# Kernel tuning notes

Measured on AMD Instinct MI355X. Metric: run time of the kernel, lower is better.

The kernel has to match this reference:

```python
import jax, jax.numpy as jnp
import numpy as np

B, S, D, H, DFF = 4, 2048, 1024, 16, 4096
DK = D // H
EPS = 1e-6


def setup_inputs() -> dict:
    key = jax.random.key(0)
    ks = jax.random.split(key, 20)
    sc = 0.02
    inp = {
        'x': jax.random.normal(ks[0], (B, S, D), jnp.float32),
        'inp_mask': jax.random.randint(ks[1], (B, 1, 1, S), 0, 2, jnp.int32),
        # linear weights stored [in, out]
        'wq_w': jax.random.normal(ks[2], (D, D), jnp.float32) * sc,
        'wq_b': jnp.zeros((D,), jnp.float32),
        'wk_w': jax.random.normal(ks[3], (D, D), jnp.float32) * sc,
        'wk_b': jnp.zeros((D,), jnp.float32),
        'wv_w': jax.random.normal(ks[4], (D, D), jnp.float32) * sc,
        'wv_b': jnp.zeros((D,), jnp.float32),
        'wo_w': jax.random.normal(ks[5], (D, D), jnp.float32) * sc,
        'wo_b': jnp.zeros((D,), jnp.float32),
        'ff_w0': jax.random.normal(ks[6], (D, DFF), jnp.float32) * sc,
        'ff_b0': jnp.zeros((DFF,), jnp.float32),
        'ff_w1': jax.random.normal(ks[7], (DFF, D), jnp.float32) * sc,
        'ff_b1': jnp.zeros((D,), jnp.float32),
        'ln0_a': jnp.ones((D,), jnp.float32),
        'ln0_b': jnp.zeros((D,), jnp.float32),
        'ln1_a': jnp.ones((D,), jnp.float32),
        'ln1_b': jnp.zeros((D,), jnp.float32),
    }
    return inp


def _layernorm(x, alpha, bias):
    # Faithful to source: unbiased std (Bessel), divide by (std + eps)
    mean = jnp.mean(x, axis=-1, keepdims=True)
    std = jnp.std(x, axis=-1, keepdims=True, ddof=1)
    return alpha * (x - mean) / (std + EPS) + bias


def _mha(x, wq_w, wq_b, wk_w, wk_b, wv_w, wv_b, wo_w, wo_b, mask):
    q = (x @ wq_w + wq_b).reshape(B, S, H, DK).transpose(0, 2, 1, 3)  # [B,H,S,DK]
    k = (x @ wk_w + wk_b).reshape(B, S, H, DK).transpose(0, 2, 1, 3)
    v = (x @ wv_w + wv_b).reshape(B, S, H, DK).transpose(0, 2, 1, 3)
    scores = jnp.einsum('bhqd,bhkd->bhqk', q, k) / jnp.sqrt(jnp.float32(DK))
    scores = jnp.where(mask == 0, jnp.float32(-1e9), scores)
    attn = jax.nn.softmax(scores, axis=-1)
    out = jnp.einsum('bhqk,bhkd->bhqd', attn, v)
    out = out.transpose(0, 2, 1, 3).reshape(B, S, D)
    return out @ wo_w + wo_b


def reference(x, inp_mask, wq_w, wq_b, wk_w, wk_b, wv_w, wv_b, wo_w, wo_b,
              ff_w0, ff_b0, ff_w1, ff_b1, ln0_a, ln0_b, ln1_a, ln1_b):
    # Residual 0: pre-norm MHA (dropout = 0)
    h = _layernorm(x, ln0_a, ln0_b)
    x = x + _mha(h, wq_w, wq_b, wk_w, wk_b, wv_w, wv_b, wo_w, wo_b, inp_mask)
    # Residual 1: pre-norm FFN
    h = _layernorm(x, ln1_a, ln1_b)
    h = jax.nn.gelu(h @ ff_w0 + ff_b0, approximate=False) @ ff_w1 + ff_b1
    return x + h
```

## Files before the change

### kernel.cpp

```cpp
#include <hip/hip_runtime.h>
#include <hip/hip_bf16.h>
#include <math.h>

#define Bc 4
#define Sc 2048
#define Dc 1024
#define Hc 16
#define DKc 64
#define DFFc 4096
#define Mc (Bc*Sc)
#define LN_EPS 1e-6f

typedef unsigned short ushort_t;
typedef short bf16x8 __attribute__((ext_vector_type(8)));
typedef float f32x4 __attribute__((ext_vector_type(4)));
typedef float f32x16 __attribute__((ext_vector_type(16)));

typedef __attribute__((address_space(3))) void lds_void_t;
typedef __attribute__((address_space(1))) const void gconst_void_t;

__device__ __forceinline__ void gload_lds16(const void* g, void* l) {
  __builtin_amdgcn_global_load_lds((gconst_void_t*)g, (lds_void_t*)l, 16, 0, 0);
}

__device__ __forceinline__ ushort_t f2bf(float f) {
  union { float f; unsigned int u; } a; a.f = f;
  unsigned int r = a.u + 0x7fffu + ((a.u >> 16) & 1u);
  return (ushort_t)(r >> 16);
}

__device__ __forceinline__ float rcpf(float x) { return __builtin_amdgcn_rcpf(x); }

__device__ __forceinline__ void swapl(unsigned& a, unsigned& b) {
  asm("v_permlane32_swap_b32 %0, %1" : "+v"(a), "+v"(b));
}
__device__ __forceinline__ unsigned cvtpk_bf16(float lo, float hi) {
  unsigned r;
  asm("v_cvt_pk_bf16_f32 %0, %1, %2" : "=v"(r) : "v"(lo), "v"(hi));
  return r;
}

__global__ __launch_bounds__(256) void k_transpose_cvt(
    const float* __restrict__ W, ushort_t* __restrict__ WT, int K, int N) {
  __shared__ float t[32][33];
  const int tx = threadIdx.x & 31, ty = threadIdx.x >> 5;
  const int n0 = blockIdx.x * 32, k0 = blockIdx.y * 32;
#pragma unroll
  for (int i = 0; i < 4; ++i)
    t[ty + i * 8][tx] = W[(size_t)(k0 + ty + i * 8) * N + n0 + tx];
  __syncthreads();
#pragma unroll
  for (int i = 0; i < 4; ++i)
    WT[(size_t)(n0 + ty + i * 8) * K + k0 + tx] = f2bf(t[tx][ty + i * 8]);
}

__global__ __launch_bounds__(256) void k_layernorm(
    const float* __restrict__ x, const float* __restrict__ alpha,
    const float* __restrict__ beta, ushort_t* __restrict__ out) {
  const int row = blockIdx.x;
  const int tid = threadIdx.x;
  const int w = tid >> 6, lane = tid & 63;
  const float4 v = ((const float4*)(x + (size_t)row * Dc))[tid];
  float s = v.x + v.y + v.z + v.w;
#pragma unroll
  for (int m = 32; m >= 1; m >>= 1) s += __shfl_xor(s, m, 64);
  __shared__ float ws[8];
  if (lane == 0) ws[w] = s;
  __syncthreads();
  s = ws[0] + ws[1] + ws[2] + ws[3];
  const float mean = s * (1.0f / Dc);
  const float dx = v.x - mean, dy = v.y - mean, dz = v.z - mean, dw = v.w - mean;
  float ss = dx * dx + dy * dy + dz * dz + dw * dw;
#pragma unroll
  for (int m = 32; m >= 1; m >>= 1) ss += __shfl_xor(ss, m, 64);
  if (lane == 0) ws[4 + w] = ss;
  __syncthreads();
  ss = ws[4] + ws[5] + ws[6] + ws[7];
  const float stdv = sqrtf(ss / (float)(Dc - 1));
  const float inv = 1.0f / (stdv + LN_EPS);
  const float4 a = ((const float4*)alpha)[tid];
  const float4 b = ((const float4*)beta)[tid];
  uint2 o;
  o.x = cvtpk_bf16(a.x * dx * inv + b.x, a.y * dy * inv + b.y);
  o.y = cvtpk_bf16(a.z * dz * inv + b.z, a.w * dw * inv + b.w);
  *(uint2*)(out + (size_t)row * Dc + tid * 4) = o;
}

__global__ __launch_bounds__(256) void k_compact(const int* __restrict__ mask,
                                                 int* __restrict__ cidx,
                                                 float* __restrict__ cmadd,
                                                 int* __restrict__ ntile) {
  const int b = blockIdx.x;
  const int tid = threadIdx.x;
  const int base = b * Sc;
  for (int i = tid; i < Sc; i += 256) cmadd[base + i] = -1.442695041e9f;
  int mloc[8];
  int cnt = 0;
#pragma unroll
  for (int j = 0; j < 8; ++j) {
    mloc[j] = mask[base + tid * 8 + j];
    cnt += mloc[j];
  }
  __shared__ int ps[256];
  ps[tid] = cnt;
  __syncthreads();
  for (int ofs = 1; ofs < 256; ofs <<= 1) {
    const int v = (tid >= ofs) ? ps[tid - ofs] : 0;
    __syncthreads();
    ps[tid] += v;
    __syncthreads();
  }
  const int total = ps[255];
  int run = tid ? ps[tid - 1] : 0;
#pragma unroll
  for (int j = 0; j < 8; ++j) {
    const int gi = base + tid * 8 + j;
    if (mloc[j]) {
      cidx[gi] = run;
      cmadd[base + run] = -8.0f;
      run++;
    } else {
      cidx[gi] = -1;
    }
  }
  if (tid == 0) {
    int nt = (total + 31) >> 5;
    ntile[b] = nt < 1 ? 1 : nt;
  }
}

template <int MODE>
__global__ __launch_bounds__(512, 4) void k_gemm8(
    const ushort_t* __restrict__ A, const ushort_t* __restrict__ BT,
    const float* __restrict__ bias, const float* __restrict__ bias2,
    const float* __restrict__ bias3, const float* __restrict__ resid,
    const int* __restrict__ cidx,
    void* __restrict__ Cout, void* __restrict__ Cout2, void* __restrict__ Cout3,
    int N, int K, int nxn ) {
  __shared__ __align__(16) ushort_t As[3][256 * 32];
  __shared__ __align__(16) ushort_t Bs[3][128 * 32];
  const int tid = threadIdx.x;
  const int lane = tid & 63;
  const int wid = tid >> 6;
  const int wm = wid >> 1, wn = wid & 1;
  const int lrow = lane & 15, lgrp = lane >> 4;
  const int xcd = blockIdx.x & 7;
  const int idx = blockIdx.x >> 3;
  const int im = xcd * 4 + (idx & 3);
  const int in_ = idx >> 2;
  const int m0 = im << 8, n0 = in_ << 7;

  const f32x4 zero4 = {0.f, 0.f, 0.f, 0.f};
  f32x4 acc[4][4];
#pragma unroll
  for (int i = 0; i < 4; ++i)
#pragma unroll
    for (int j = 0; j < 4; ++j) acc[i][j] = zero4;

  const int ar0 = tid >> 2;
  const int as0 = (tid & 3) ^ ((ar0 >> 1) & 3);
  const int ar1 = ar0 + 128;
  const ushort_t* Ag0 = A + (size_t)(m0 + ar0) * K + as0 * 8;
  const ushort_t* Ag1 = A + (size_t)(m0 + ar1) * K + as0 * 8;
  const ushort_t* Bg0 = BT + (size_t)(n0 + ar0 % 128) * K + as0 * 8;
  char* const a_w = (char*)(&As[0][0]) + wid * 1024;
  char* const b_w = (char*)(&Bs[0][0]) + wid * 1024;

  const int sl = lgrp ^ ((lrow >> 1) & 3);
  const int aoff = (wm * 64 + lrow) * 32 + sl * 8;
  const int boff = (wn * 64 + lrow) * 32 + sl * 8;

  const int nk = K >> 5;
  {
    gload_lds16(Ag0, a_w);
    gload_lds16(Ag1, a_w + 8192);
    gload_lds16(Bg0, b_w);
    gload_lds16(Ag0 + 32, a_w + 16384);
    gload_lds16(Ag1 + 32, a_w + 16384 + 8192);
    gload_lds16(Bg0 + 32, b_w + 8192);
  }
  int cur = 0;
  for (int t = 0; t < nk; ++t) {
    if (t + 1 < nk) { asm volatile("s_waitcnt vmcnt(3)" ::: "memory"); }
    else            { asm volatile("s_waitcnt vmcnt(0)" ::: "memory"); }
    asm volatile("s_barrier" ::: "memory");
    const ushort_t* Ab = &As[cur][0];
    const ushort_t* Bb = &Bs[cur][0];
    bf16x8 af[4], bf[4];
#pragma unroll
    for (int mf = 0; mf < 4; ++mf) af[mf] = *(const bf16x8*)(Ab + aoff + mf * 512);
#pragma unroll
    for (int nf = 0; nf < 4; ++nf) bf[nf] = *(const bf16x8*)(Bb + boff + nf * 512);
    if (t + 2 < nk) {
      const int bi = (cur + 2 >= 3) ? cur - 1 : cur + 2;
      const size_t ko = (size_t)(t + 2) * 32;
      gload_lds16(Ag0 + ko, a_w + bi * 16384);
      gload_lds16(Ag1 + ko, a_w + bi * 16384 + 8192);
      gload_lds16(Bg0 + ko, b_w + bi * 8192);
    }
    __builtin_amdgcn_s_setprio(1);
#pragma unroll
    for (int mf = 0; mf < 4; ++mf)
#pragma unroll
      for (int nf = 0; nf < 4; ++nf)
        acc[mf][nf] = __builtin_amdgcn_mfma_f32_16x16x32_bf16(af[mf], bf[nf], acc[mf][nf], 0, 0, 0);
    __builtin_amdgcn_s_setprio(0);
    asm volatile("s_barrier" ::: "memory");
    cur = (cur + 1 == 3) ? 0 : cur + 1;
  }

  const float* bsrc = bias;
  int n0l = n0;
  int seg = 0;
  if (MODE == 4) {
    seg = n0 >> 10;
    n0l = n0 & 1023;
    bsrc = (seg == 0) ? bias : (seg == 1 ? bias2 : bias3);
  }
  float bv[4];
#pragma unroll
  for (int n = 0; n < 4; ++n) bv[n] = bsrc[n0l + wn * 64 + n * 16 + lrow];

  const int gb = m0 >> 11;

#pragma unroll
  for (int m = 0; m < 4; ++m) {
    int cpv[4];
    if (MODE == 4 && seg >= 1) {
#pragma unroll
      for (int r = 0; r < 4; ++r)
        cpv[r] = cidx[m0 + wm * 64 + m * 16 + lgrp * 4 + r];
    }
#pragma unroll
    for (int n = 0; n < 4; ++n) {
      const int col = (MODE == 4 ? n0l : n0) + wn * 64 + n * 16 + lrow;
      if (MODE == 4 && seg == 2) {
        const int hh = col >> 6, dd = col & 63;
        ushort_t* Cv = (ushort_t*)Cout3 + ((size_t)(gb * Hc + hh) * DKc + dd) * Sc;
#pragma unroll
        for (int r = 0; r < 4; r += 2) {
          const unsigned wpk = cvtpk_bf16(acc[m][n][r] + bv[n], acc[m][n][r + 1] + bv[n]);
          if (cpv[r] >= 0) Cv[cpv[r]] = (ushort_t)wpk;
          if (cpv[r + 1] >= 0) Cv[cpv[r + 1]] = (ushort_t)(wpk >> 16);
        }
      } else if (MODE == 4 && seg == 1) {
        ushort_t* Ck = (ushort_t*)Cout2 + (size_t)gb * Sc * Dc + col;
#pragma unroll
        for (int r = 0; r < 4; r += 2) {
          const unsigned wpk = cvtpk_bf16(acc[m][n][r] + bv[n], acc[m][n][r + 1] + bv[n]);
          if (cpv[r] >= 0) Ck[(size_t)cpv[r] * Dc] = (ushort_t)wpk;
          if (cpv[r + 1] >= 0) Ck[(size_t)cpv[r + 1] * Dc] = (ushort_t)(wpk >> 16);
        }
      } else if (MODE == 4) {
        ushort_t* Co = (ushort_t*)Cout;
        const size_t row0 = (size_t)(m0 + wm * 64 + m * 16 + lgrp * 4);
#pragma unroll
        for (int r = 0; r < 4; r += 2) {
          const unsigned wpk = cvtpk_bf16(acc[m][n][r] + bv[n], acc[m][n][r + 1] + bv[n]);
          Co[(row0 + r) * Dc + col] = (ushort_t)wpk;
          Co[(row0 + r + 1) * Dc + col] = (ushort_t)(wpk >> 16);
        }
      } else if (MODE == 2) {
        const size_t row0 = (size_t)(m0 + wm * 64 + m * 16 + lgrp * 4);
#pragma unroll
        for (int r = 0; r < 4; r += 2) {
          float v0 = acc[m][n][r] + bv[n];
          float v1 = acc[m][n][r + 1] + bv[n];
          v0 = v0 * rcpf(1.0f + exp2f(-2.4554669f * v0));
          v1 = v1 * rcpf(1.0f + exp2f(-2.4554669f * v1));
          const unsigned wpk = cvtpk_bf16(v0, v1);
          ((ushort_t*)Cout)[(row0 + r) * N + col] = (ushort_t)wpk;
          ((ushort_t*)Cout)[(row0 + r + 1) * N + col] = (ushort_t)(wpk >> 16);
        }
      } else {
#pragma unroll
        for (int r = 0; r < 4; ++r) {
          const size_t row = (size_t)(m0 + wm * 64 + m * 16 + lgrp * 4 + r);
          const float v = acc[m][n][r] + bv[n] + resid[row * N + col];
          ((float*)Cout)[row * N + col] = v;
        }
      }
    }
  }
}

#define KSCALE 0.1803368801e0f
__global__ __launch_bounds__(512) void k_attn12(
    const ushort_t* __restrict__ Qb, const ushort_t* __restrict__ Kb,
    const ushort_t* __restrict__ Vt, const float* __restrict__ madd,
    const int* __restrict__ ntile, ushort_t* __restrict__ Ob) {
  __shared__ __align__(16) ushort_t Ks[4][32 * 64];
  __shared__ __align__(16) ushort_t Vs[4][64 * 32];
  __shared__ __align__(16) float Ms[Sc];

  const int bid = blockIdx.x;
  const int xcd = bid & 7, idx = bid >> 3;
  const int bh = xcd * 8 + (idx >> 3);
  const int qb = idx & 7;
  const int b = bh >> 4, h = bh & 15;
  const int nt = ntile[b];
  const int tid = threadIdx.x;
  const int lane = tid & 63, w = tid >> 6;
  const int l31 = lane & 31, hi = lane >> 5;
  const size_t bS = (size_t)b * Sc;
  const int qrow0 = qb * 256 + w * 32;

  bf16x8 qf[4];
  const ushort_t* qp = Qb + (bS + qrow0 + l31) * Dc + h * DKc + hi * 8;
#pragma unroll
  for (int c = 0; c < 4; ++c) qf[c] = *(const bf16x8*)(qp + c * 16);

  bf16x8 ones;
#pragma unroll
  for (int i = 0; i < 8; ++i) ones[i] = (short)0x3F80;

  f32x16 accA, accB, accS;
#pragma unroll
  for (int i = 0; i < 16; ++i) { accA[i] = 0.f; accB[i] = 0.f; accS[i] = 0.f; }

  const ushort_t* Vth = Vt + (size_t)bh * (DKc * Sc);
  const float* mp = madd + b * Sc;

  const int c0 = tid & 255;
  const int kr = c0 >> 3, ksl = (c0 & 7) ^ (kr & 7);
  const int vr = c0 >> 2, vsl = (c0 & 3) ^ ((vr >> 1) & 3);
  const ushort_t* Kg = Kb + (bS + kr) * Dc + h * DKc + ksl * 8;
  const ushort_t* Vg = Vth + (size_t)vr * Sc + vsl * 8;
  char* const k_w = (char*)(&Ks[0][0]) + (w & 3) * 1024;
  char* const v_w = (char*)(&Vs[0][0]) + (w & 3) * 1024;

  gload_lds16(mp + tid * 4, (char*)Ms + w * 1024);
  if (w < 4) {
    gload_lds16(Kg, k_w);
    gload_lds16(Kg + (size_t)32 * Dc, k_w + 4096);
  } else {
    gload_lds16(Vg, v_w);
    gload_lds16(Vg + 32, v_w + 4096);
  }

  const int vsw = (l31 >> 1) & 3;
  int cur = 0;
  f32x16 scA, scB;

  auto qk_phase = [&](f32x16& scN, int t) {
    const char* Kbuf = (const char*)(&Ks[cur][0]);
    bf16x8 kf[4];
#pragma unroll
    for (int c = 0; c < 4; ++c) {
      const int slr = (c * 2 + hi) ^ (l31 & 7);
      kf[c] = *(const bf16x8*)(Kbuf + l31 * 128 + slr * 16);
    }
    if (t + 2 < 64) {
      const int bi = (cur + 2) & 3;
      const size_t kv2 = (size_t)(t + 2) * 32;
      if (w < 4) gload_lds16(Kg + kv2 * Dc, k_w + bi * 4096);
      else       gload_lds16(Vg + kv2, v_w + bi * 4096);
    }
#pragma unroll
    for (int i = 0; i < 16; ++i) scN[i] = 0.f;
    __builtin_amdgcn_s_setprio(1);
    scN = __builtin_amdgcn_mfma_f32_32x32x16_bf16(kf[0], qf[0], scN, 0, 0, 0);
    scN = __builtin_amdgcn_mfma_f32_32x32x16_bf16(kf[1], qf[1], scN, 0, 0, 0);
    scN = __builtin_amdgcn_mfma_f32_32x32x16_bf16(kf[2], qf[2], scN, 0, 0, 0);
    scN = __builtin_amdgcn_mfma_f32_32x32x16_bf16(kf[3], qf[3], scN, 0, 0, 0);
    __builtin_amdgcn_s_setprio(0);
  };

  auto sm_pv = [&](f32x16& scP, int tp) {
    float4 mv[4];
#pragma unroll
    for (int c = 0; c < 4; ++c)
      mv[c] = *(const float4*)(&Ms[tp * 32 + c * 8 + 4 * hi]);
    const char* Vbuf = (const char*)(&Vs[(cur + 3) & 3][0]);
    const bf16x8 v00 = *(const bf16x8*)(Vbuf + l31 * 64 + ((hi ^ vsw) * 16));
    const bf16x8 v01 = *(const bf16x8*)(Vbuf + l31 * 64 + (((2 + hi) ^ vsw) * 16));
    const bf16x8 v10 = *(const bf16x8*)(Vbuf + (32 + l31) * 64 + ((hi ^ vsw) * 16));
    const bf16x8 v11 = *(const bf16x8*)(Vbuf + (32 + l31) * 64 + (((2 + hi) ^ vsw) * 16));
    float p[16];
    p[0] = exp2f(scP[0] * KSCALE + mv[0].x);  p[1] = exp2f(scP[1] * KSCALE + mv[0].y);
    p[2] = exp2f(scP[2] * KSCALE + mv[0].z);  p[3] = exp2f(scP[3] * KSCALE + mv[0].w);
    p[4] = exp2f(scP[4] * KSCALE + mv[1].x);  p[5] = exp2f(scP[5] * KSCALE + mv[1].y);
    p[6] = exp2f(scP[6] * KSCALE + mv[1].z);  p[7] = exp2f(scP[7] * KSCALE + mv[1].w);
    p[8] = exp2f(scP[8] * KSCALE + mv[2].x);  p[9] = exp2f(scP[9] * KSCALE + mv[2].y);
    p[10] = exp2f(scP[10] * KSCALE + mv[2].z); p[11] = exp2f(scP[11] * KSCALE + mv[2].w);
    p[12] = exp2f(scP[12] * KSCALE + mv[3].x); p[13] = exp2f(scP[13] * KSCALE + mv[3].y);
    p[14] = exp2f(scP[14] * KSCALE + mv[3].z); p[15] = exp2f(scP[15] * KSCALE + mv[3].w);
    unsigned cw[4][2];
#pragma unroll
    for (int a = 0; a < 4; ++a) {
      cw[a][0] = cvtpk_bf16(p[4 * a + 0], p[4 * a + 1]);
      cw[a][1] = cvtpk_bf16(p[4 * a + 2], p[4 * a + 3]);
    }
    unsigned a00 = cw[0][0], b00 = cw[1][0]; swapl(a00, b00);
    unsigned a01 = cw[0][1], b01 = cw[1][1]; swapl(a01, b01);
    unsigned a10 = cw[2][0], b10 = cw[3][0]; swapl(a10, b10);
    unsigned a11 = cw[2][1], b11 = cw[3][1]; swapl(a11, b11);
    union { unsigned u[4]; bf16x8 v; } pa0, pa1;
    pa0.u[0] = a00; pa0.u[1] = a01; pa0.u[2] = b00; pa0.u[3] = b01;
    pa1.u[0] = a10; pa1.u[1] = a11; pa1.u[2] = b10; pa1.u[3] = b11;
    __builtin_amdgcn_s_setprio(1);
    accA = __builtin_amdgcn_mfma_f32_32x32x16_bf16(pa0.v, v00, accA, 0, 0, 0);
    accA = __builtin_amdgcn_mfma_f32_32x32x16_bf16(pa1.v, v01, accA, 0, 0, 0);
    accB = __builtin_amdgcn_mfma_f32_32x32x16_bf16(pa0.v, v10, accB, 0, 0, 0);
    accB = __builtin_amdgcn_mfma_f32_32x32x16_bf16(pa1.v, v11, accB, 0, 0, 0);
    accS = __builtin_amdgcn_mfma_f32_32x32x16_bf16(pa0.v, ones, accS, 0, 0, 0);
    accS = __builtin_amdgcn_mfma_f32_32x32x16_bf16(pa1.v, ones, accS, 0, 0, 0);
    __builtin_amdgcn_s_setprio(0);
  };

  asm volatile("s_waitcnt vmcnt(1)" ::: "memory");
  asm volatile("s_barrier" ::: "memory");
  qk_phase(scA, 0);
  cur = 1;
  int t = 1;
  for (; t + 1 < nt; t += 2) {
    asm volatile("s_waitcnt vmcnt(1)" ::: "memory");
    asm volatile("s_barrier" ::: "memory");
    qk_phase(scB, t);
    sm_pv(scA, t - 1);
    cur = (cur + 1) & 3;
    asm volatile("s_waitcnt vmcnt(1)" ::: "memory");
    asm volatile("s_barrier" ::: "memory");
    qk_phase(scA, t + 1);
    sm_pv(scB, t);
    cur = (cur + 1) & 3;
  }
  if (t < nt) {
    asm volatile("s_waitcnt vmcnt(1)" ::: "memory");
    asm volatile("s_barrier" ::: "memory");
    qk_phase(scB, t);
    sm_pv(scA, t - 1);
    cur = (cur + 1) & 3;
    asm volatile("s_waitcnt vmcnt(0)" ::: "memory");
    sm_pv(scB, t);
  } else {
    asm volatile("s_waitcnt vmcnt(0)" ::: "memory");
    sm_pv(scA, nt - 1);
  }

#pragma unroll
  for (int r = 0; r < 16; ++r) {
    const int q = (r & 3) + 8 * (r >> 2) + 4 * hi;
    const float inv = rcpf(accS[r]);
    ushort_t* op = Ob + (bS + qrow0 + q) * Dc + h * DKc + l31;
    op[0] = f2bf(accA[r] * inv);
    op[32] = f2bf(accB[r] * inv);
  }
}

extern "C" void kernel_launch(void* const* d_in, const int* in_sizes, int n_in,
                              void* d_out, int out_size, void* d_ws, size_t ws_size,
                              hipStream_t stream) {
  const float* x     = (const float*)d_in[0];
  const int* mask    = (const int*)d_in[1];
  const float* wq_w  = (const float*)d_in[2];
  const float* wq_b  = (const float*)d_in[3];
  const float* wk_w  = (const float*)d_in[4];
  const float* wk_b  = (const float*)d_in[5];
  const float* wv_w  = (const float*)d_in[6];
  const float* wv_b  = (const float*)d_in[7];
  const float* wo_w  = (const float*)d_in[8];
  const float* wo_b  = (const float*)d_in[9];
  const float* ff_w0 = (const float*)d_in[10];
  const float* ff_b0 = (const float*)d_in[11];
  const float* ff_w1 = (const float*)d_in[12];
  const float* ff_b1 = (const float*)d_in[13];
  const float* ln0_a = (const float*)d_in[14];
  const float* ln0_b = (const float*)d_in[15];
  const float* ln1_a = (const float*)d_in[16];
  const float* ln1_b = (const float*)d_in[17];
  float* out = (float*)d_out;

  char* ws = (char*)d_ws;
  size_t off = 0;
  ushort_t* WTq = (ushort_t*)(ws + off); off += (size_t)Dc * Dc * 2;
  ushort_t* WTk = (ushort_t*)(ws + off); off += (size_t)Dc * Dc * 2;
  ushort_t* WTv = (ushort_t*)(ws + off); off += (size_t)Dc * Dc * 2;
  ushort_t* WTo = (ushort_t*)(ws + off); off += (size_t)Dc * Dc * 2;
  ushort_t* WT0 = (ushort_t*)(ws + off); off += (size_t)DFFc * Dc * 2;
  ushort_t* WT1 = (ushort_t*)(ws + off); off += (size_t)Dc * DFFc * 2;
  ushort_t* hbuf = (ushort_t*)(ws + off); off += (size_t)Mc * Dc * 2;
  ushort_t* qbuf = (ushort_t*)(ws + off); off += (size_t)Mc * Dc * 2;
  ushort_t* kbuf = (ushort_t*)(ws + off); off += (size_t)Mc * Dc * 2;
  ushort_t* vtb  = (ushort_t*)(ws + off); off += (size_t)Mc * Dc * 2;
  ushort_t* abuf = (ushort_t*)(ws + off); off += (size_t)Mc * Dc * 2;
  float* maddb   = (float*)(ws + off);   off += (size_t)Bc * Sc * 4;
  int* cidxb     = (int*)(ws + off);     off += (size_t)Mc * 4;
  int* ntileb    = (int*)(ws + off);     off += 64;
  ushort_t* gbuf = qbuf;

  const dim3 blk(256);
  const dim3 blk512(512);
  k_transpose_cvt<<<dim3(Dc / 32, Dc / 32), blk, 0, stream>>>(wq_w, WTq, Dc, Dc);
  k_transpose_cvt<<<dim3(Dc / 32, Dc / 32), blk, 0, stream>>>(wk_w, WTk, Dc, Dc);
  k_transpose_cvt<<<dim3(Dc / 32, Dc / 32), blk, 0, stream>>>(wv_w, WTv, Dc, Dc);
  k_transpose_cvt<<<dim3(Dc / 32, Dc / 32), blk, 0, stream>>>(wo_w, WTo, Dc, Dc);
  k_transpose_cvt<<<dim3(DFFc / 32, Dc / 32), blk, 0, stream>>>(ff_w0, WT0, Dc, DFFc);
  k_transpose_cvt<<<dim3(Dc / 32, DFFc / 32), blk, 0, stream>>>(ff_w1, WT1, DFFc, Dc);
  k_compact<<<dim3(Bc), blk, 0, stream>>>(mask, cidxb, maddb, ntileb);
  k_layernorm<<<Mc, blk, 0, stream>>>(x, ln0_a, ln0_b, hbuf);
  k_gemm8<4><<<dim3(768), blk512, 0, stream>>>(hbuf, WTq, wq_b, wk_b, wv_b, nullptr,
                                               cidxb, qbuf, kbuf, vtb, 3072, Dc, 3);
  k_attn12<<<dim3(512), blk512, 0, stream>>>(qbuf, kbuf, vtb, maddb, ntileb, abuf);
  k_gemm8<1><<<dim3(256), blk512, 0, stream>>>(abuf, WTo, wo_b, nullptr, nullptr, x,
                                               nullptr, out, nullptr, nullptr, Dc, Dc, 1);
  k_layernorm<<<Mc, blk, 0, stream>>>(out, ln1_a, ln1_b, hbuf);
  k_gemm8<2><<<dim3(1024), blk512, 0, stream>>>(hbuf, WT0, ff_b0, nullptr, nullptr, nullptr,
                                                nullptr, gbuf, nullptr, nullptr, DFFc, Dc, 4);
  k_gemm8<1><<<dim3(256), blk512, 0, stream>>>(gbuf, WT1, ff_b1, nullptr, nullptr, out,
                                               nullptr, out, nullptr, nullptr, Dc, DFFc, 1);
}
```

Before: 370.7 us.

## Add dedicated 4-stage pipelined GEMM kernel for residual output projections

Adds a specialized k_gemm8d kernel for the two N=1024 GEMMs with a residual add (the attention output projection and the second FFN projection). It uses a 4-buffer LDS ring with three k-tiles prefetched through global_load_lds, explicit vmcnt waits, s_setprio around the MFMA block, and launch_bounds(512,2) so two blocks can share a CU. The goal is to hide global-load latency better than the generic templated kernel for these skinny-N shapes. The cost is a larger LDS footprint (96KB per block) and a separate kernel to maintain, and the in-place resid==Cout call is only safe because each element is read before it is written by the same thread.

```diff
diff --git a/kernel.cpp b/kernel.cpp
--- a/kernel.cpp
+++ b/kernel.cpp
@@ -282,6 +282,97 @@
       }
     }
   }
+}
+
+__global__ __launch_bounds__(512, 2) void k_gemm8d(
+    const ushort_t* __restrict__ A, const ushort_t* __restrict__ BT,
+    const float* __restrict__ bias, const float* __restrict__ resid,
+    float* __restrict__ Cout, int N, int K) {
+  __shared__ __align__(16) ushort_t As[4][256 * 32];
+  __shared__ __align__(16) ushort_t Bs[4][128 * 32];
+  const int tid = threadIdx.x;
+  const int lane = tid & 63;
+  const int wid = tid >> 6;
+  const int wm = wid >> 1, wn = wid & 1;
+  const int lrow = lane & 15, lgrp = lane >> 4;
+  const int xcd = blockIdx.x & 7;
+  const int idx = blockIdx.x >> 3;
+  const int im = xcd * 4 + (idx & 3);
+  const int in_ = idx >> 2;
+  const int m0 = im << 8, n0 = in_ << 7;
+
+  const f32x4 zero4 = {0.f, 0.f, 0.f, 0.f};
+  f32x4 acc[4][4];
+#pragma unroll
+  for (int i = 0; i < 4; ++i)
+#pragma unroll
+    for (int j = 0; j < 4; ++j) acc[i][j] = zero4;
+
+  const int ar0 = tid >> 2;
+  const int as0 = (tid & 3) ^ ((ar0 >> 1) & 3);
+  const int ar1 = ar0 + 128;
+  const ushort_t* Ag0 = A + (size_t)(m0 + ar0) * K + as0 * 8;
+  const ushort_t* Ag1 = A + (size_t)(m0 + ar1) * K + as0 * 8;
+  const ushort_t* Bg0 = BT + (size_t)(n0 + ar0 % 128) * K + as0 * 8;
+  char* const a_w = (char*)(&As[0][0]) + wid * 1024;
+  char* const b_w = (char*)(&Bs[0][0]) + wid * 1024;
+
+  const int sl = lgrp ^ ((lrow >> 1) & 3);
+  const int aoff = (wm * 64 + lrow) * 32 + sl * 8;
+  const int boff = (wn * 64 + lrow) * 32 + sl * 8;
+
+  const int nk = K >> 5;
+#pragma unroll
+  for (int tt = 0; tt < 3; ++tt) {
+    const size_t ko = (size_t)tt * 32;
+    gload_lds16(Ag0 + ko, a_w + tt * 16384);
+    gload_lds16(Ag1 + ko, a_w + tt * 16384 + 8192);
+    gload_lds16(Bg0 + ko, b_w + tt * 8192);
+  }
+  int cur = 0;
+  for (int t = 0; t < nk; ++t) {
+    if (t + 2 < nk)      { asm volatile("s_waitcnt vmcnt(6)" ::: "memory"); }
+    else if (t + 1 < nk) { asm volatile("s_waitcnt vmcnt(3)" ::: "memory"); }
+    else                 { asm volatile("s_waitcnt vmcnt(0)" ::: "memory"); }
+    asm volatile("s_barrier" ::: "memory");
+    const ushort_t* Ab = &As[cur][0];
+    const ushort_t* Bb = &Bs[cur][0];
+    bf16x8 af[4], bf[4];
+#pragma unroll
+    for (int mf = 0; mf < 4; ++mf) af[mf] = *(const bf16x8*)(Ab + aoff + mf * 512);
+#pragma unroll
+    for (int nf = 0; nf < 4; ++nf) bf[nf] = *(const bf16x8*)(Bb + boff + nf * 512);
+    if (t + 3 < nk) {
+      const int bi = (cur + 3) & 3;
+      const size_t ko = (size_t)(t + 3) * 32;
+      gload_lds16(Ag0 + ko, a_w + bi * 16384);
+      gload_lds16(Ag1 + ko, a_w + bi * 16384 + 8192);
+      gload_lds16(Bg0 + ko, b_w + bi * 8192);
+    }
+    __builtin_amdgcn_s_setprio(1);
+#pragma unroll
+    for (int mf = 0; mf < 4; ++mf)
+#pragma unroll
+      for (int nf = 0; nf < 4; ++nf)
+        acc[mf][nf] = __builtin_amdgcn_mfma_f32_16x16x32_bf16(af[mf], bf[nf], acc[mf][nf], 0, 0, 0);
+    __builtin_amdgcn_s_setprio(0);
+    asm volatile("s_barrier" ::: "memory");
+    cur = (cur + 1) & 3;
+  }
+
+  float bv[4];
+#pragma unroll
+  for (int n = 0; n < 4; ++n) bv[n] = bias[n0 + wn * 64 + n * 16 + lrow];
+#pragma unroll
+  for (int m = 0; m < 4; ++m)
+#pragma unroll
+    for (int n = 0; n < 4; ++n)
+#pragma unroll
+      for (int r = 0; r < 4; ++r) {
+        const size_t row = (size_t)(m0 + wm * 64 + m * 16 + lgrp * 4 + r);
+        const size_t col = (size_t)(n0 + wn * 64 + n * 16 + lrow);
+        Cout[row * N + col] = acc[m][n][r] + bv[n] + resid[row * N + col];
+      }
 }
 
 #define KSCALE 0.1803368801e0f
@@ -502,11 +593,9 @@
   k_gemm8<4><<<dim3(768), blk512, 0, stream>>>(hbuf, WTq, wq_b, wk_b, wv_b, nullptr,
                                                cidxb, qbuf, kbuf, vtb, 3072, Dc, 3);
   k_attn12<<<dim3(512), blk512, 0, stream>>>(qbuf, kbuf, vtb, maddb, ntileb, abuf);
-  k_gemm8<1><<<dim3(256), blk512, 0, stream>>>(abuf, WTo, wo_b, nullptr, nullptr, x,
-                                               nullptr, out, nullptr, nullptr, Dc, Dc, 1);
+  k_gemm8d<<<dim3(256), blk512, 0, stream>>>(abuf, WTo, wo_b, x, out, Dc, Dc);
   k_layernorm<<<Mc, blk, 0, stream>>>(out, ln1_a, ln1_b, hbuf);
   k_gemm8<2><<<dim3(1024), blk512, 0, stream>>>(hbuf, WT0, ff_b0, nullptr, nullptr, nullptr,
                                                 nullptr, gbuf, nullptr, nullptr, DFFc, Dc, 4);
-  k_gemm8<1><<<dim3(256), blk512, 0, stream>>>(gbuf, WT1, ff_b1, nullptr, nullptr, out,
-                                               nullptr, out, nullptr, nullptr, Dc, DFFc, 1);
-}
+  k_gemm8d<<<dim3(256), blk512, 0, stream>>>(gbuf, WT1, ff_b1, out, out, Dc, DFFc);
+}
```

Result: no change. 370.8 us (+0.0%).
